# Optimization experiments

Measured on AMD Instinct MI355X. Metric: run time of the kernel, lower is better.

Reference implementation:

```python
import math
import jax, jax.numpy as jnp
import numpy as np

B, S, D, H, DK = 2, 2048, 1024, 16, 64
NUM_BUCKETS, MAX_DISTANCE = 32, 128


def _relative_position_bucket(rel_pos):
    # bidirectional=True (encoder): is_decoder=False
    nb = NUM_BUCKETS // 2
    rel_buckets = (rel_pos > 0).astype(jnp.int32) * nb
    rp = jnp.abs(rel_pos)
    max_exact = nb // 2
    is_small = rp < max_exact
    rp_large = max_exact + (
        jnp.log(rp.astype(jnp.float32) / max_exact)
        / math.log(MAX_DISTANCE / max_exact)
        * (nb - max_exact)
    ).astype(jnp.int32)
    rp_large = jnp.minimum(rp_large, nb - 1)
    return rel_buckets + jnp.where(is_small, rp, rp_large)


def compute_bias(rel_bias, q_len, k_len):
    ctx = jnp.arange(q_len, dtype=jnp.int32)[:, None]
    mem = jnp.arange(k_len, dtype=jnp.int32)[None, :]
    buckets = _relative_position_bucket(mem - ctx)          # [q,k]
    vals = rel_bias[buckets]                                 # [q,k,H]
    return jnp.transpose(vals, (2, 0, 1))[None]              # [1,H,q,k]


def setup_inputs() -> dict:
    key = jax.random.key(0)
    ks = jax.random.split(key, 6)
    scale = 0.02
    return {
        "hidden_states": jax.random.normal(ks[0], (B, S, D), jnp.float32),
        "Wq": jax.random.normal(ks[1], (D, H * DK), jnp.float32) * scale,
        "Wk": jax.random.normal(ks[2], (D, H * DK), jnp.float32) * scale,
        "Wv": jax.random.normal(ks[3], (D, H * DK), jnp.float32) * scale,
        "Wo": jax.random.normal(ks[4], (H * DK, D), jnp.float32) * scale,
        "rel_bias": jax.random.normal(ks[5], (NUM_BUCKETS, H), jnp.float32) * scale,
    }


def reference(hidden_states, Wq, Wk, Wv, Wo, rel_bias):
    b, s, _ = hidden_states.shape

    def shape(x):  # [b,s,H*DK] -> [b,H,s,DK]
        return x.reshape(b, s, H, DK).transpose(0, 2, 1, 3)

    q = shape(hidden_states @ Wq)
    k = shape(hidden_states @ Wk)
    v = shape(hidden_states @ Wv)

    # T5: no 1/sqrt(d_k) scaling
    scores = jnp.einsum("bhqd,bhkd->bhqk", q, k)
    position_bias = compute_bias(rel_bias, s, s)             # [1,H,s,s]
    scores = scores + position_bias
    attn = jax.nn.softmax(scores.astype(jnp.float32), axis=-1).astype(scores.dtype)
    out = jnp.einsum("bhqk,bhkd->bhqd", attn, v)
    out = out.transpose(0, 2, 1, 3).reshape(b, s, H * DK)
    return out @ Wo
```

## Files before the change

### kernel.cpp

```cpp
#include <hip/hip_runtime.h>

#define HH 16
#define DKK 64
#define SS 2048
#define BB 2
#define DD 1024

typedef __attribute__((ext_vector_type(4))) float f32x4;
typedef __attribute__((ext_vector_type(8))) short bf16x8;
typedef __attribute__((ext_vector_type(4))) short s16x4;
typedef __attribute__((ext_vector_type(2))) int i32x2;

__device__ __forceinline__ short bf16b(float f) {
    union { float f; unsigned u; } x; x.f = f;
    unsigned r = (x.u + 0x7fffu + ((x.u >> 16) & 1u)) >> 16;
    return (short)r;
}

__device__ __forceinline__ unsigned f2u(float f) {
    union { float f; unsigned u; } x; x.f = f;
    return x.u;
}

__device__ __forceinline__ f32x4 mfma16(bf16x8 a, bf16x8 b, f32x4 c) {
    return __builtin_amdgcn_mfma_f32_16x16x32_bf16(a, b, c, 0, 0, 0);
}

__device__ __forceinline__ void lds16(const short* g, short* l) {
    __builtin_amdgcn_global_load_lds(
        (const __attribute__((address_space(1))) void*)g,
        (__attribute__((address_space(3))) void*)l, 16, 0, 0);
}

__global__ __launch_bounds__(256) void cvt_bf16(const float* __restrict__ x,
                                                short* __restrict__ y, int n) {
    int i = (blockIdx.x * 256 + threadIdx.x) * 4;
    if (i >= n) return;
    f32x4 v = *(const f32x4*)(x + i);
    s16x4 o;
    o.x = bf16b(v.x); o.y = bf16b(v.y); o.z = bf16b(v.z); o.w = bf16b(v.w);
    *(s16x4*)(y + i) = o;
}

__global__ __launch_bounds__(256) void transpose_w(
    const float* __restrict__ W0, const float* __restrict__ W1,
    const float* __restrict__ W2, const float* __restrict__ W3,
    short* __restrict__ T0, short* __restrict__ T1,
    short* __restrict__ T2, short* __restrict__ T3) {
    const float* W; short* T;
    switch (blockIdx.z) {
        case 0: W = W0; T = T0; break;
        case 1: W = W1; T = T1; break;
        case 2: W = W2; T = T2; break;
        default: W = W3; T = T3; break;
    }
    __shared__ short tile[32][33];
    int n0 = blockIdx.x * 32, k0 = blockIdx.y * 32;
    int tx = threadIdx.x & 31;
    int ty = (threadIdx.x >> 5) * 4;
#pragma unroll
    for (int i = 0; i < 4; i++)
        tile[ty + i][tx] = bf16b(W[(k0 + ty + i) * DD + n0 + tx]);
    __syncthreads();
#pragma unroll
    for (int i = 0; i < 4; i++)
        T[(n0 + ty + i) * DD + k0 + tx] = tile[tx][ty + i];
}

__global__ __launch_bounds__(256) void build_bias(const float* __restrict__ rb,
                                                  float* __restrict__ tab) {
    int idx = blockIdx.x * 256 + threadIdx.x;
    if (idx >= HH * 4095) return;
    int h = idx / 4095, d = idx % 4095;
    int rel = d - 2047;
    int bucket = (rel > 0) ? 16 : 0;
    unsigned r = (rel < 0) ? (unsigned)(-rel) : (unsigned)rel;
    int add;
    if (r < 8) add = (int)r;
    else {
        int e = 31 - __clz(r);
        unsigned long long r2 = (unsigned long long)r * (unsigned long long)r;
        int f = 2 * e + ((r2 >= (2ull << (2 * e))) ? 1 : 0);
        add = 8 + (f - 6);
        if (add > 15) add = 15;
    }
    bucket += add;
    tab[h * 4095 + d] = rb[bucket * HH + h] * 1.44269504f;
}

__global__ __launch_bounds__(256) void gemm_qkv(
    const short* __restrict__ A, const short* __restrict__ Wt,
    short* __restrict__ Cq, short* __restrict__ Ck, short* __restrict__ Cvt) {
    const int K = 1024;
    __shared__ short As[128 * 32];
    __shared__ short Bs[128 * 32];
    int tid = threadIdx.x;
    int wave = tid >> 6, lane = tid & 63;
    int quad = lane >> 4, l16 = lane & 15;
    int m0 = blockIdx.y * 128, n0 = blockIdx.x * 128;

    int wm = (wave & 1) * 64, wn = (wave >> 1) * 64;
    int r0 = tid >> 2, c0 = (tid & 3) * 8;

    f32x4 acc[4][4];
#pragma unroll
    for (int i = 0; i < 4; i++)
#pragma unroll
        for (int j = 0; j < 4; j++) acc[i][j] = (f32x4){0.f, 0.f, 0.f, 0.f};

    for (int k0 = 0; k0 < K; k0 += 32) {
        __syncthreads();
        lds16(A + (size_t)(m0 + r0) * K + k0 + c0, As + wave * 512);
        lds16(A + (size_t)(m0 + 64 + r0) * K + k0 + c0, As + 2048 + wave * 512);
        lds16(Wt + (size_t)(n0 + r0) * K + k0 + c0, Bs + wave * 512);
        lds16(Wt + (size_t)(n0 + 64 + r0) * K + k0 + c0, Bs + 2048 + wave * 512);
        __syncthreads();
        bf16x8 af[4], bfr[4];
#pragma unroll
        for (int t = 0; t < 4; t++) {
            af[t] = *(const bf16x8*)(As + (wm + t * 16 + l16) * 32 + quad * 8);
            bfr[t] = *(const bf16x8*)(Bs + (wn + t * 16 + l16) * 32 + quad * 8);
        }
#pragma unroll
        for (int mt = 0; mt < 4; mt++)
#pragma unroll
            for (int nt = 0; nt < 4; nt++)
                acc[mt][nt] = mfma16(af[mt], bfr[nt], acc[mt][nt]);
    }

#pragma unroll
    for (int mt = 0; mt < 4; mt++) {
#pragma unroll
        for (int nt = 0; nt < 4; nt++) {
#pragma unroll
            for (int r = 0; r < 4; r++) {
                int gm = m0 + wm + mt * 16 + quad * 4 + r;
                int gn = n0 + wn + nt * 16 + l16;
                int b = gm >> 11, s = gm & 2047;
                int which = gn >> 10;
                int h = (gn >> 6) & 15, dk = gn & 63;
                short bv = bf16b(acc[mt][nt][r]);
                if (which == 0)
                    Cq[(((size_t)(b * HH + h)) * SS + s) * DKK + dk] = bv;
                else if (which == 1)
                    Ck[(((size_t)(b * HH + h)) * SS + s) * DKK + dk] = bv;
                else
                    Cvt[(((size_t)(b * HH + h)) * DKK + dk) * SS + s] = bv;
            }
        }
    }
}

__global__ __launch_bounds__(256) void gemm_out(
    const short* __restrict__ A, const short* __restrict__ Wt,
    float* __restrict__ Cout) {
    const int K = 1024, N = 1024;
    __shared__ short As[64 * 32];
    __shared__ short Bs[128 * 32];
    int tid = threadIdx.x;
    int wave = tid >> 6, lane = tid & 63;
    int quad = lane >> 4, l16 = lane & 15;
    int m0 = blockIdx.y * 64, n0 = blockIdx.x * 128;

    int wm = (wave & 1) * 32, wn = (wave >> 1) * 64;
    int r0 = tid >> 2, c0 = (tid & 3) * 8;

    f32x4 acc[2][4];
#pragma unroll
    for (int i = 0; i < 2; i++)
#pragma unroll
        for (int j = 0; j < 4; j++) acc[i][j] = (f32x4){0.f, 0.f, 0.f, 0.f};

    for (int k0 = 0; k0 < K; k0 += 32) {
        __syncthreads();
        lds16(A + (size_t)(m0 + r0) * K + k0 + c0, As + wave * 512);
        lds16(Wt + (size_t)(n0 + r0) * K + k0 + c0, Bs + wave * 512);
        lds16(Wt + (size_t)(n0 + 64 + r0) * K + k0 + c0, Bs + 2048 + wave * 512);
        __syncthreads();
        bf16x8 af[2], bfr[4];
#pragma unroll
        for (int t = 0; t < 2; t++)
            af[t] = *(const bf16x8*)(As + (wm + t * 16 + l16) * 32 + quad * 8);
#pragma unroll
        for (int t = 0; t < 4; t++)
            bfr[t] = *(const bf16x8*)(Bs + (wn + t * 16 + l16) * 32 + quad * 8);
#pragma unroll
        for (int mt = 0; mt < 2; mt++)
#pragma unroll
            for (int nt = 0; nt < 4; nt++)
                acc[mt][nt] = mfma16(af[mt], bfr[nt], acc[mt][nt]);
    }

#pragma unroll
    for (int mt = 0; mt < 2; mt++)
#pragma unroll
        for (int nt = 0; nt < 4; nt++)
#pragma unroll
            for (int r = 0; r < 4; r++) {
                int gm = m0 + wm + mt * 16 + quad * 4 + r;
                int gn = n0 + wn + nt * 16 + l16;
                Cout[(size_t)gm * N + gn] = acc[mt][nt][r];
            }
}

__global__ __launch_bounds__(256, 2) void attn(
    const short* __restrict__ Q, const short* __restrict__ Kmat,
    const short* __restrict__ Vt, const float* __restrict__ btab,
    short* __restrict__ O) {
    __shared__ short Ks[2][64 * 64];
    __shared__ short Vs[2][64 * 64];
    __shared__ float bias_s[2176];
    __shared__ short P_s[4][2][16 * 64];

    int tid = threadIdx.x;
    int wave = tid >> 6, lane = tid & 63;
    int quad = lane >> 4, l16 = lane & 15;
    int bh = blockIdx.x;
    int h = bh & 15, b = bh >> 4;
    int q0b = blockIdx.y * 128;
    int q0w = q0b + wave * 32;

    const short* Qb = Q + (size_t)bh * SS * DKK;
    const short* Kb = Kmat + (size_t)bh * SS * DKK;
    const short* Vb = Vt + (size_t)bh * DKK * SS;
    const float* bt = btab + h * 4095;

    int woff = 1920 - q0b;
    for (int i = tid; i < 2176; i += 256) {
        int gi = woff + i;
        bias_s[i] = bt[gi > 4094 ? 4094 : gi];
    }
    float blo = bt[2047 - 128];
    float bhi = bt[2047 + 128];

    int kro = tid >> 3;
    int gk = (tid & 7) ^ (kro & 7);
    const short* Kg0 = Kb + (size_t)kro * DKK + gk * 8;
    const short* Kg1 = Kb + (size_t)(kro + 32) * DKK + gk * 8;
    const short* Vg0 = Vb + (size_t)kro * SS + gk * 8;
    const short* Vg1 = Vb + (size_t)(kro + 32) * SS + gk * 8;

    bf16x8 qf[2][2];
#pragma unroll
    for (int qs = 0; qs < 2; qs++) {
        qf[qs][0] = *(const bf16x8*)(Qb + (q0w + qs * 16 + l16) * DKK + quad * 8);
        qf[qs][1] = *(const bf16x8*)(Qb + (q0w + qs * 16 + l16) * DKK + 32 + quad * 8);
    }

    f32x4 o[2][4];
#pragma unroll
    for (int qs = 0; qs < 2; qs++)
#pragma unroll
        for (int i = 0; i < 4; i++) o[qs][i] = (f32x4){0.f, 0.f, 0.f, 0.f};
    f32x4 lacc[2];
    lacc[0] = (f32x4){0.f, 0.f, 0.f, 0.f};
    lacc[1] = (f32x4){0.f, 0.f, 0.f, 0.f};

    bf16x8 onesf;
    short onev = (l16 == 0) ? (short)0x3F80 : (short)0;
#pragma unroll
    for (int i = 0; i < 8; i++) onesf[i] = onev;

    short* Pw = &P_s[wave][0][0];
    int gxor = l16 & 7;
    int ghalf = quad >> 1;
    int wbase = l16 * 64 + (quad & 1) * 4;
    int ra0 = l16 * 64 + ((quad ^ gxor) * 8);
    int ra1 = l16 * 64 + (((4 + quad) ^ gxor) * 8);
    int bidx = 127 + quad * 4 - wave * 32 - l16;
    int sl0 = (quad ^ gxor) * 8;
    int sl1 = ((4 + quad) ^ gxor) * 8;

    lds16(Kg0, &Ks[0][wave * 512]);
    lds16(Kg1, &Ks[0][2048 + wave * 512]);
    lds16(Vg0, &Vs[0][wave * 512]);
    lds16(Vg1, &Vs[0][2048 + wave * 512]);

    int cur = 0;
    for (int kc = 0; kc < SS; kc += 64) {
        __syncthreads();
        int kn = (kc + 64) & (SS - 1);
        int nxt = cur ^ 1;
        lds16(Kg0 + (size_t)kn * DKK, &Ks[nxt][wave * 512]);
        lds16(Kg1 + (size_t)kn * DKK, &Ks[nxt][2048 + wave * 512]);
        lds16(Vg0 + kn, &Vs[nxt][wave * 512]);
        lds16(Vg1 + kn, &Vs[nxt][2048 + wave * 512]);

        float breg[2][16];
#pragma unroll
        for (int qs = 0; qs < 2; qs++) {
            int q0s = q0w + qs * 16;
            if (kc > q0s - 191 && kc < q0s + 143) {
#pragma unroll
                for (int kt = 0; kt < 4; kt++)
#pragma unroll
                    for (int r = 0; r < 4; r++)
                        breg[qs][kt * 4 + r] =
                            bias_s[bidx + kc + kt * 16 + r - qs * 16];
            } else {
                float bc = (kc <= q0s - 191) ? blo : bhi;
#pragma unroll
                for (int i = 0; i < 16; i++) breg[qs][i] = bc;
            }
        }

        const short* Ksc = &Ks[cur][0];
        const short* Vsc = &Vs[cur][0];

        f32x4 s[2][4];
#pragma unroll
        for (int kt = 0; kt < 4; kt++) {
            int row = (kt * 16 + l16) * 64;
            bf16x8 kf0 = *(const bf16x8*)(Ksc + row + sl0);
            bf16x8 kf1 = *(const bf16x8*)(Ksc + row + sl1);
            s[0][kt] = mfma16(kf0, qf[0][0], (f32x4){0.f, 0.f, 0.f, 0.f});
            s[0][kt] = mfma16(kf1, qf[0][1], s[0][kt]);
            s[1][kt] = mfma16(kf0, qf[1][0], (f32x4){0.f, 0.f, 0.f, 0.f});
            s[1][kt] = mfma16(kf1, qf[1][1], s[1][kt]);
        }
        bf16x8 vf[4][2];
#pragma unroll
        for (int nt = 0; nt < 4; nt++) {
            int row = (nt * 16 + l16) * 64;
            vf[nt][0] = *(const bf16x8*)(Vsc + row + sl0);
            vf[nt][1] = *(const bf16x8*)(Vsc + row + sl1);
        }

#pragma unroll
        for (int qs = 0; qs < 2; qs++) {
#pragma unroll
            for (int kt = 0; kt < 4; kt++) {
                unsigned u[4];
#pragma unroll
                for (int r = 0; r < 4; r++) {
                    float p = __builtin_amdgcn_exp2f(
                        fmaf(s[qs][kt][r], 1.44269504f, breg[qs][kt * 4 + r]));
                    u[r] = f2u(p) + 0x8000u;
                }
                unsigned d0 = __builtin_amdgcn_perm(u[1], u[0], 0x07060302u);
                unsigned d1 = __builtin_amdgcn_perm(u[3], u[2], 0x07060302u);
                int g = (kt * 2 + ghalf) ^ gxor;
                *(i32x2*)(Pw + qs * 1024 + wbase + g * 8) = (i32x2){(int)d0, (int)d1};
            }
        }
        __asm__ __volatile__("" ::: "memory");
#pragma unroll
        for (int qs = 0; qs < 2; qs++) {
            bf16x8 pf0 = *(const bf16x8*)(Pw + qs * 1024 + ra0);
            bf16x8 pf1 = *(const bf16x8*)(Pw + qs * 1024 + ra1);
            lacc[qs] = mfma16(pf0, onesf, lacc[qs]);
            lacc[qs] = mfma16(pf1, onesf, lacc[qs]);
#pragma unroll
            for (int nt = 0; nt < 4; nt++) {
                o[qs][nt] = mfma16(pf0, vf[nt][0], o[qs][nt]);
                o[qs][nt] = mfma16(pf1, vf[nt][1], o[qs][nt]);
            }
        }
        __asm__ __volatile__("" ::: "memory");
        cur ^= 1;
    }

#pragma unroll
    for (int qs = 0; qs < 2; qs++) {
        float inv[4];
#pragma unroll
        for (int r = 0; r < 4; r++) {
            float l = __shfl(lacc[qs][r], lane & 48);
            inv[r] = 1.f / l;
        }
#pragma unroll
        for (int nt = 0; nt < 4; nt++)
#pragma unroll
            for (int r = 0; r < 4; r++) {
                int qrow = q0w + qs * 16 + quad * 4 + r;
                int dk = nt * 16 + l16;
                O[((size_t)(b * SS + qrow)) * (HH * DKK) + h * DKK + dk] =
                    bf16b(o[qs][nt][r] * inv[r]);
            }
    }
}

extern "C" void kernel_launch(void* const* d_in, const int* in_sizes, int n_in,
                              void* d_out, int out_size, void* d_ws, size_t ws_size,
                              hipStream_t stream) {
    const float* hs = (const float*)d_in[0];
    const float* Wq = (const float*)d_in[1];
    const float* Wk = (const float*)d_in[2];
    const float* Wv = (const float*)d_in[3];
    const float* Wo = (const float*)d_in[4];
    const float* rb = (const float*)d_in[5];
    float* out = (float*)d_out;

    char* ws = (char*)d_ws;
    size_t off = 0;
    auto alloc = [&](size_t bytes) -> void* {
        void* p = (void*)(ws + off);
        off += (bytes + 255) & ~(size_t)255;
        return p;
    };
    const size_t M = (size_t)BB * SS;
    short* hsb = (short*)alloc(M * DD * 2);
    short* WqT = (short*)alloc((size_t)DD * DD * 2);
    short* WkT = (short*)alloc((size_t)DD * DD * 2);
    short* WvT = (short*)alloc((size_t)DD * DD * 2);
    short* WoT = (short*)alloc((size_t)DD * DD * 2);
    short* Qb  = (short*)alloc(M * DD * 2);
    short* Kb  = (short*)alloc(M * DD * 2);
    short* VTb = (short*)alloc(M * DD * 2);
    short* Ab  = (short*)alloc(M * DD * 2);
    float* btab = (float*)alloc((size_t)HH * 4095 * 4);

    int nHS = (int)(M * DD);
    cvt_bf16<<<nHS / 1024, 256, 0, stream>>>(hs, hsb, nHS);
    transpose_w<<<dim3(32, 32, 4), 256, 0, stream>>>(Wq, Wk, Wv, Wo, WqT, WkT, WvT, WoT);
    build_bias<<<(HH * 4095 + 255) / 256, 256, 0, stream>>>(rb, btab);
    gemm_qkv<<<dim3(24, 32), 256, 0, stream>>>(hsb, WqT, Qb, Kb, VTb);
    attn<<<dim3(32, 16), 256, 0, stream>>>(Qb, Kb, VTb, btab, Ab);
    gemm_out<<<dim3(8, 64), 256, 0, stream>>>(Ab, WoT, out);
}
```

Baseline: 196.3 us.

## Double GEMM K-step per barrier and store attention bias in bf16 for occupancy

Both projection GEMMs now stage a 64-wide K slice per iteration as two 32-wide panels. This halves the number of __syncthreads round-trips and issues more global-to-LDS loads per barrier. The attention kernel stores its shared relative-bias window as bf16 instead of fp32, which cuts that buffer's LDS footprint, and raises the launch-bounds occupancy hint from 2 to 3 blocks per CU. The trade-offs are less precise bias values near the diagonal, while the clamped far-range values stay fp32, plus doubled GEMM LDS usage and possible register pressure under the tighter occupancy bound.

```diff
diff --git a/kernel.cpp b/kernel.cpp
--- a/kernel.cpp
+++ b/kernel.cpp
@@ -15,6 +15,12 @@
     union { float f; unsigned u; } x; x.f = f;
     unsigned r = (x.u + 0x7fffu + ((x.u >> 16) & 1u)) >> 16;
     return (short)r;
+}
+
+__device__ __forceinline__ float b2f(short s) {
+    union { unsigned u; float f; } x;
+    x.u = ((unsigned)(unsigned short)s) << 16;
+    return x.f;
 }
 
 __device__ __forceinline__ unsigned f2u(float f) {
@@ -92,8 +98,8 @@
     const short* __restrict__ A, const short* __restrict__ Wt,
     short* __restrict__ Cq, short* __restrict__ Ck, short* __restrict__ Cvt) {
     const int K = 1024;
-    __shared__ short As[128 * 32];
-    __shared__ short Bs[128 * 32];
+    __shared__ short As[128 * 64];
+    __shared__ short Bs[128 * 64];
     int tid = threadIdx.x;
     int wave = tid >> 6, lane = tid & 63;
     int quad = lane >> 4, l16 = lane & 15;
@@ -108,24 +114,33 @@
 #pragma unroll
         for (int j = 0; j < 4; j++) acc[i][j] = (f32x4){0.f, 0.f, 0.f, 0.f};
 
-    for (int k0 = 0; k0 < K; k0 += 32) {
+    for (int k0 = 0; k0 < K; k0 += 64) {
         __syncthreads();
-        lds16(A + (size_t)(m0 + r0) * K + k0 + c0, As + wave * 512);
-        lds16(A + (size_t)(m0 + 64 + r0) * K + k0 + c0, As + 2048 + wave * 512);
-        lds16(Wt + (size_t)(n0 + r0) * K + k0 + c0, Bs + wave * 512);
-        lds16(Wt + (size_t)(n0 + 64 + r0) * K + k0 + c0, Bs + 2048 + wave * 512);
+#pragma unroll
+        for (int p = 0; p < 2; p++) {
+            int kp = k0 + p * 32;
+            lds16(A + (size_t)(m0 + r0) * K + kp + c0, As + p * 4096 + wave * 512);
+            lds16(A + (size_t)(m0 + 64 + r0) * K + kp + c0,
+                  As + p * 4096 + 2048 + wave * 512);
+            lds16(Wt + (size_t)(n0 + r0) * K + kp + c0, Bs + p * 4096 + wave * 512);
+            lds16(Wt + (size_t)(n0 + 64 + r0) * K + kp + c0,
+                  Bs + p * 4096 + 2048 + wave * 512);
+        }
         __syncthreads();
-        bf16x8 af[4], bfr[4];
-#pragma unroll
-        for (int t = 0; t < 4; t++) {
-            af[t] = *(const bf16x8*)(As + (wm + t * 16 + l16) * 32 + quad * 8);
-            bfr[t] = *(const bf16x8*)(Bs + (wn + t * 16 + l16) * 32 + quad * 8);
-        }
-#pragma unroll
-        for (int mt = 0; mt < 4; mt++)
-#pragma unroll
-            for (int nt = 0; nt < 4; nt++)
-                acc[mt][nt] = mfma16(af[mt], bfr[nt], acc[mt][nt]);
+#pragma unroll
+        for (int p = 0; p < 2; p++) {
+            bf16x8 af[4], bfr[4];
+#pragma unroll
+            for (int t = 0; t < 4; t++) {
+                af[t] = *(const bf16x8*)(As + p * 4096 + (wm + t * 16 + l16) * 32 + quad * 8);
+                bfr[t] = *(const bf16x8*)(Bs + p * 4096 + (wn + t * 16 + l16) * 32 + quad * 8);
+            }
+#pragma unroll
+            for (int mt = 0; mt < 4; mt++)
+#pragma unroll
+                for (int nt = 0; nt < 4; nt++)
+                    acc[mt][nt] = mfma16(af[mt], bfr[nt], acc[mt][nt]);
+        }
     }
 
 #pragma unroll
@@ -155,8 +170,8 @@
     const short* __restrict__ A, const short* __restrict__ Wt,
     float* __restrict__ Cout) {
     const int K = 1024, N = 1024;
-    __shared__ short As[64 * 32];
-    __shared__ short Bs[128 * 32];
+    __shared__ short As[64 * 64];
+    __shared__ short Bs[128 * 64];
     int tid = threadIdx.x;
     int wave = tid >> 6, lane = tid & 63;
     int quad = lane >> 4, l16 = lane & 15;
@@ -171,24 +186,32 @@
 #pragma unroll
         for (int j = 0; j < 4; j++) acc[i][j] = (f32x4){0.f, 0.f, 0.f, 0.f};
 
-    for (int k0 = 0; k0 < K; k0 += 32) {
+    for (int k0 = 0; k0 < K; k0 += 64) {
         __syncthreads();
-        lds16(A + (size_t)(m0 + r0) * K + k0 + c0, As + wave * 512);
-        lds16(Wt + (size_t)(n0 + r0) * K + k0 + c0, Bs + wave * 512);
-        lds16(Wt + (size_t)(n0 + 64 + r0) * K + k0 + c0, Bs + 2048 + wave * 512);
+#pragma unroll
+        for (int p = 0; p < 2; p++) {
+            int kp = k0 + p * 32;
+            lds16(A + (size_t)(m0 + r0) * K + kp + c0, As + p * 2048 + wave * 512);
+            lds16(Wt + (size_t)(n0 + r0) * K + kp + c0, Bs + p * 4096 + wave * 512);
+            lds16(Wt + (size_t)(n0 + 64 + r0) * K + kp + c0,
+                  Bs + p * 4096 + 2048 + wave * 512);
+        }
         __syncthreads();
-        bf16x8 af[2], bfr[4];
-#pragma unroll
-        for (int t = 0; t < 2; t++)
-            af[t] = *(const bf16x8*)(As + (wm + t * 16 + l16) * 32 + quad * 8);
-#pragma unroll
-        for (int t = 0; t < 4; t++)
-            bfr[t] = *(const bf16x8*)(Bs + (wn + t * 16 + l16) * 32 + quad * 8);
-#pragma unroll
-        for (int mt = 0; mt < 2; mt++)
-#pragma unroll
-            for (int nt = 0; nt < 4; nt++)
-                acc[mt][nt] = mfma16(af[mt], bfr[nt], acc[mt][nt]);
+#pragma unroll
+        for (int p = 0; p < 2; p++) {
+            bf16x8 af[2], bfr[4];
+#pragma unroll
+            for (int t = 0; t < 2; t++)
+                af[t] = *(const bf16x8*)(As + p * 2048 + (wm + t * 16 + l16) * 32 + quad * 8);
+#pragma unroll
+            for (int t = 0; t < 4; t++)
+                bfr[t] = *(const bf16x8*)(Bs + p * 4096 + (wn + t * 16 + l16) * 32 + quad * 8);
+#pragma unroll
+            for (int mt = 0; mt < 2; mt++)
+#pragma unroll
+                for (int nt = 0; nt < 4; nt++)
+                    acc[mt][nt] = mfma16(af[mt], bfr[nt], acc[mt][nt]);
+        }
     }
 
 #pragma unroll
@@ -203,13 +226,13 @@
             }
 }
 
-__global__ __launch_bounds__(256, 2) void attn(
+__global__ __launch_bounds__(256, 3) void attn(
     const short* __restrict__ Q, const short* __restrict__ Kmat,
     const short* __restrict__ Vt, const float* __restrict__ btab,
     short* __restrict__ O) {
     __shared__ short Ks[2][64 * 64];
     __shared__ short Vs[2][64 * 64];
-    __shared__ float bias_s[2176];
+    __shared__ short bias_s[2176];
     __shared__ short P_s[4][2][16 * 64];
 
     int tid = threadIdx.x;
@@ -228,7 +251,7 @@
     int woff = 1920 - q0b;
     for (int i = tid; i < 2176; i += 256) {
         int gi = woff + i;
-        bias_s[i] = bt[gi > 4094 ? 4094 : gi];
+        bias_s[i] = bf16b(bt[gi > 4094 ? 4094 : gi]);
     }
     float blo = bt[2047 - 128];
     float bhi = bt[2047 + 128];
@@ -296,7 +319,7 @@
 #pragma unroll
                     for (int r = 0; r < 4; r++)
                         breg[qs][kt * 4 + r] =
-                            bias_s[bidx + kc + kt * 16 + r - qs * 16];
+                            b2f(bias_s[bidx + kc + kt * 16 + r - qs * 16]);
             } else {
                 float bc = (kc <= q0s - 191) ? blo : bhi;
 #pragma unroll
```

New measurement: 212.1 us. +8.1%, slower.
